# Kernel optimization log

Measured on AMD Instinct MI355X. Metric: run time of the kernel, lower is better.

Reference implementation:

```python
import jax, jax.numpy as jnp
import numpy as np

N_NODES = 50000
D = 128
N_EDGES = 600000


def setup_inputs() -> dict:
    key = jax.random.key(0)
    k_h, k_u, k_v, k_s, k_d = jax.random.split(key, 5)
    H = jax.random.normal(k_h, (N_NODES, D), dtype=jnp.float32)
    U = jax.random.normal(k_u, (D, D), dtype=jnp.float32)
    V = jax.random.normal(k_v, (D, D), dtype=jnp.float32)
    edge_src = jax.random.randint(k_s, (N_EDGES,), 0, N_NODES, dtype=jnp.int32)
    edge_dst = jax.random.randint(k_d, (N_EDGES,), 0, N_NODES, dtype=jnp.int32)
    return {"H": H, "U": U, "V": V, "edge_src": edge_src, "edge_dst": edge_dst}


def reference(H, U, V, edge_src, edge_dst):
    # Synchronous form of: new_rep[n] = relu(rep[n] @ U + sum_{m in N(n)} rep[m] @ V)
    # Compute H @ V once (one dense GEMM), then irregular gather by edge_src
    # and segment-sum scatter into destination nodes.
    hv = H @ V                                    # [N, D]
    msgs = jnp.take(hv, edge_src, axis=0)         # [E, D] irregular gather
    agg = jax.ops.segment_sum(msgs, edge_dst, num_segments=H.shape[0])  # [N, D]
    return jax.nn.relu(H @ U + agg)               # [N, D]
```

## Files before the change

### kernel.cpp

```cpp
#include <hip/hip_runtime.h>
#include <hip/hip_bf16.h>

constexpr int kNodes  = 50000;
constexpr int kEdges  = 600000;
constexpr int kD      = 128;
constexpr int kStrips = kNodes / 16;
constexpr int kStride = 64;

constexpr int kNB        = 400;
constexpr int kNPB       = 125;
constexpr int kEPB       = 4096;
constexpr int kBktBlocks = (kEdges + kEPB - 1) / kEPB;
constexpr int kCellCap   = 32;
constexpr int kCellStr   = 148;
constexpr int kPackBlocks  = 128;
constexpr int kPrepBlocks  = kBktBlocks + kPackBlocks;
constexpr int kGemmBlocks  = 768;
constexpr int kK2Blocks    = kNB + kGemmBlocks;

typedef __attribute__((ext_vector_type(8))) short  short8;
typedef __attribute__((ext_vector_type(4))) float  f32x4;

__device__ __forceinline__ unsigned short f2bfu(float x) {
    __hip_bfloat16 h = __float2bfloat16(x);
    return (unsigned short)__builtin_bit_cast(short, h);
}
__device__ __forceinline__ short f2bf(float x) {
    return __builtin_bit_cast(short, __float2bfloat16(x));
}

__global__ __launch_bounds__(256) void prep(const float* __restrict__ U,
                                            const float* __restrict__ V,
                                            const int* __restrict__ esrc,
                                            const int* __restrict__ edst,
                                            short* __restrict__ BTf,
                                            unsigned short* __restrict__ cnt_arr,
                                            unsigned int* __restrict__ barr) {
    const int bid = blockIdx.x;

    if (bid < kBktBlocks) {
        __shared__ int cur[kNB];
        for (int i = threadIdx.x; i < kNB; i += 256) cur[i] = 0;
        __syncthreads();

        const int e0 = bid * kEPB;
        int myd[16], mys[16];
#pragma unroll
        for (int i = 0; i < 16; ++i) {
            const int e = e0 + i * 256 + (int)threadIdx.x;
            myd[i] = (e < kEdges) ? edst[e] : -1;
            mys[i] = (e < kEdges) ? esrc[e] : 0;
        }
#pragma unroll
        for (int i = 0; i < 16; ++i) {
            if (myd[i] >= 0) {
                const int b = myd[i] / kNPB;
                const int slot = atomicAdd(&cur[b], 1);
                if (slot < kCellCap)
                    barr[((size_t)bid * kNB + b) * kCellCap + slot] =
                        ((unsigned)(myd[i] - b * kNPB) << 16) | (unsigned)mys[i];
            }
        }
        __syncthreads();
        for (int i = threadIdx.x; i < kNB; i += 256)
            cnt_arr[(size_t)i * kCellStr + bid] =
                (unsigned short)min(cur[i], kCellCap);
        return;
    }

    const int g = (bid - kBktBlocks) * 256 + (int)threadIdx.x;
    const int c = g >> 7;
    const int k = g & 127;
    const float x = (c < kD) ? U[k * kD + c] : V[k * kD + (c - kD)];
    const int q  = c >> 6;
    const int n  = (c >> 4) & 3;
    const int m  = c & 15;
    const int t  = k >> 5;
    const int kg = (k >> 3) & 3;
    const int ko = k & 7;
    const int lane = kg * 16 + m;
    BTf[((((q * 4 + n) * 4 + t) * 64 + lane) << 3) + ko] = f2bf(x);
}

__global__ __launch_bounds__(256) void gemm_sort(const float* __restrict__ H,
                                                 const short* __restrict__ BTf,
                                                 const unsigned short* __restrict__ cnt_arr,
                                                 const unsigned int* __restrict__ barr,
                                                 unsigned short* __restrict__ outb,
                                                 unsigned short* __restrict__ hvb,
                                                 int* __restrict__ cursor,
                                                 unsigned short* __restrict__ csr16) {
    const int bid = blockIdx.x;

    if (bid < kNB) {
        __shared__ int cnt[kNPB];
        for (int i = threadIdx.x; i < kNPB; i += 256) cnt[i] = 0;
        __syncthreads();

        const int b = bid;
        const int t = (int)threadIdx.x;
        if (t < kBktBlocks) {
            const int c = cnt_arr[(size_t)b * kCellStr + t];
            const unsigned int* cell = barr + ((size_t)t * kNB + b) * kCellCap;
            for (int j = 0; j < c; ++j) {
                const unsigned int p = cell[j];
                const int dl  = (int)(p >> 16);
                const int src = (int)(p & 0xffffu);
                const int slot = atomicAdd(&cnt[dl], 1);
                if (slot < kStride)
                    csr16[((size_t)b * kNPB + dl) * kStride + slot] = (unsigned short)src;
            }
        }
        __syncthreads();
        for (int i = threadIdx.x; i < kNPB; i += 256)
            cursor[b * kNPB + i] = cnt[i];
        return;
    }

    const int g  = bid - kNB;
    const int s0 = (int)((long)g       * kStrips / kGemmBlocks);
    const int s1 = (int)((long)(g + 1) * kStrips / kGemmBlocks);
    const int quad = threadIdx.x >> 6;
    const int lane = threadIdx.x & 63;
    const int m  = lane & 15;
    const int kg = lane >> 4;

    const short8* bq = reinterpret_cast<const short8*>(BTf)
                     + ((size_t)quad * 16) * 64 + lane;
    short8 bf[4][4];
#pragma unroll
    for (int n = 0; n < 4; ++n)
#pragma unroll
        for (int t = 0; t < 4; ++t)
            bf[n][t] = bq[(n * 4 + t) * 64];

    auto load_ha = [&](int s, float4 (&ha)[4][2]) {
        const float* hbase = H + ((long)s * 16 + m) * kD + kg * 8;
#pragma unroll
        for (int t = 0; t < 4; ++t) {
            ha[t][0] = *reinterpret_cast<const float4*>(hbase + t * 32);
            ha[t][1] = *reinterpret_cast<const float4*>(hbase + t * 32 + 4);
        }
    };

    auto compute_store = [&](int s, float4 (&ha)[4][2]) {
        short8 a[4];
#pragma unroll
        for (int t = 0; t < 4; ++t) {
            a[t][0] = f2bf(ha[t][0].x); a[t][1] = f2bf(ha[t][0].y);
            a[t][2] = f2bf(ha[t][0].z); a[t][3] = f2bf(ha[t][0].w);
            a[t][4] = f2bf(ha[t][1].x); a[t][5] = f2bf(ha[t][1].y);
            a[t][6] = f2bf(ha[t][1].z); a[t][7] = f2bf(ha[t][1].w);
        }

        f32x4 acc[4];
#pragma unroll
        for (int i = 0; i < 4; ++i) acc[i] = (f32x4){0.f, 0.f, 0.f, 0.f};
#pragma unroll
        for (int t = 0; t < 4; ++t)
#pragma unroll
            for (int n = 0; n < 4; ++n)
                acc[n] = __builtin_amdgcn_mfma_f32_16x16x32_bf16(bf[n][t], a[t], acc[n], 0, 0, 0);

        const long row0 = (long)s * 16;
        if (quad < 2) {
            unsigned short* rowp = outb + (size_t)(row0 + m) * 256 + quad * 64 + kg * 4;
#pragma unroll
            for (int n = 0; n < 4; ++n) {
                uint2 pk;
                pk.x = ((unsigned)f2bfu(acc[n][1]) << 16) | f2bfu(acc[n][0]);
                pk.y = ((unsigned)f2bfu(acc[n][3]) << 16) | f2bfu(acc[n][2]);
                *reinterpret_cast<uint2*>(rowp + n * 16) = pk;
            }
        } else {
            unsigned short* rowp = hvb + (size_t)(row0 + m) * kD + (quad - 2) * 64 + kg * 4;
#pragma unroll
            for (int n = 0; n < 4; ++n) {
                uint2 pk;
                pk.x = ((unsigned)f2bfu(acc[n][1]) << 16) | f2bfu(acc[n][0]);
                pk.y = ((unsigned)f2bfu(acc[n][3]) << 16) | f2bfu(acc[n][2]);
                *reinterpret_cast<uint2*>(rowp + n * 16) = pk;
            }
        }
    };

    float4 haA[4][2], haB[4][2];
    int s = s0;
    if (s >= s1) return;
    load_ha(s, haA);
    for (; s + 1 < s1; s += 2) {
        load_ha(s + 1, haB);
        compute_store(s, haA);
        if (s + 2 < s1) load_ha(s + 2, haA);
        compute_store(s + 1, haB);
    }
    if (s < s1) compute_store(s, haA);
}

__global__ __launch_bounds__(256) void aggregate_relu(const unsigned int* __restrict__ hvb,
                                                      const int* __restrict__ cursor,
                                                      const unsigned short* __restrict__ csr16,
                                                      float* __restrict__ out) {
    const int wid  = (int)((blockIdx.x * (long)blockDim.x + threadIdx.x) >> 6);
    const int lane = threadIdx.x & 63;
    if (wid >= kNodes) return;

    const unsigned int hw = reinterpret_cast<const unsigned int*>(out)[(size_t)wid * 128 + lane];
    const int deg = min(cursor[wid], kStride);
    const unsigned int w =
        reinterpret_cast<const unsigned int*>(csr16 + (size_t)wid * kStride)[lane & 31];

    float a0 = 0.f, a1 = 0.f;
    int e = 0;
    for (; e + 8 <= deg; e += 8) {
        const int p0 = __builtin_amdgcn_readlane(w, (e >> 1));
        const int p1 = __builtin_amdgcn_readlane(w, (e >> 1) + 1);
        const int p2 = __builtin_amdgcn_readlane(w, (e >> 1) + 2);
        const int p3 = __builtin_amdgcn_readlane(w, (e >> 1) + 3);
        const unsigned int w0 = hvb[(size_t)(p0 & 0xffff) * 64 + lane];
        const unsigned int w1 = hvb[(size_t)((p0 >> 16) & 0xffff) * 64 + lane];
        const unsigned int w2 = hvb[(size_t)(p1 & 0xffff) * 64 + lane];
        const unsigned int w3 = hvb[(size_t)((p1 >> 16) & 0xffff) * 64 + lane];
        const unsigned int w4 = hvb[(size_t)(p2 & 0xffff) * 64 + lane];
        const unsigned int w5 = hvb[(size_t)((p2 >> 16) & 0xffff) * 64 + lane];
        const unsigned int w6 = hvb[(size_t)(p3 & 0xffff) * 64 + lane];
        const unsigned int w7 = hvb[(size_t)((p3 >> 16) & 0xffff) * 64 + lane];
        a0 += __uint_as_float(w0 << 16) + __uint_as_float(w1 << 16)
            + __uint_as_float(w2 << 16) + __uint_as_float(w3 << 16)
            + __uint_as_float(w4 << 16) + __uint_as_float(w5 << 16)
            + __uint_as_float(w6 << 16) + __uint_as_float(w7 << 16);
        a1 += __uint_as_float(w0 & 0xffff0000u) + __uint_as_float(w1 & 0xffff0000u)
            + __uint_as_float(w2 & 0xffff0000u) + __uint_as_float(w3 & 0xffff0000u)
            + __uint_as_float(w4 & 0xffff0000u) + __uint_as_float(w5 & 0xffff0000u)
            + __uint_as_float(w6 & 0xffff0000u) + __uint_as_float(w7 & 0xffff0000u);
    }
    for (; e + 4 <= deg; e += 4) {
        const int p0 = __builtin_amdgcn_readlane(w, e >> 1);
        const int p1 = __builtin_amdgcn_readlane(w, (e >> 1) + 1);
        const unsigned int w0 = hvb[(size_t)(p0 & 0xffff) * 64 + lane];
        const unsigned int w1 = hvb[(size_t)((p0 >> 16) & 0xffff) * 64 + lane];
        const unsigned int w2 = hvb[(size_t)(p1 & 0xffff) * 64 + lane];
        const unsigned int w3 = hvb[(size_t)((p1 >> 16) & 0xffff) * 64 + lane];
        a0 += __uint_as_float(w0 << 16) + __uint_as_float(w1 << 16)
            + __uint_as_float(w2 << 16) + __uint_as_float(w3 << 16);
        a1 += __uint_as_float(w0 & 0xffff0000u) + __uint_as_float(w1 & 0xffff0000u)
            + __uint_as_float(w2 & 0xffff0000u) + __uint_as_float(w3 & 0xffff0000u);
    }
    for (; e < deg; ++e) {
        const int p = __builtin_amdgcn_readlane(w, e >> 1);
        const int s = (e & 1) ? ((p >> 16) & 0xffff) : (p & 0xffff);
        const unsigned int wv = hvb[(size_t)s * 64 + lane];
        a0 += __uint_as_float(wv << 16);
        a1 += __uint_as_float(wv & 0xffff0000u);
    }

    const float b0 = __uint_as_float(hw << 16);
    const float b1 = __uint_as_float(hw & 0xffff0000u);

    float2* out2 = reinterpret_cast<float2*>(out);
    float2 o;
    o.x = fmaxf(b0 + a0, 0.f);
    o.y = fmaxf(b1 + a1, 0.f);
    out2[(size_t)wid * 64 + lane] = o;
}

extern "C" void kernel_launch(void* const* d_in, const int* in_sizes, int n_in,
                              void* d_out, int out_size, void* d_ws, size_t ws_size,
                              hipStream_t stream) {
    const float* H    = (const float*)d_in[0];
    const float* U    = (const float*)d_in[1];
    const float* V    = (const float*)d_in[2];
    const int*   esrc = (const int*)d_in[3];
    const int*   edst = (const int*)d_in[4];

    float* out = (float*)d_out;

    char* p = (char*)d_ws;
    unsigned short* hvb     = (unsigned short*)p;  p += (size_t)kNodes * kD * 2;
    short*          BTf     = (short*)p;           p += (size_t)256 * kD * 2;
    unsigned short* cnt_arr = (unsigned short*)p;  p += (size_t)kNB * kCellStr * 2;
    unsigned int*   barr    = (unsigned int*)p;    p += (size_t)kBktBlocks * kNB * kCellCap * 4;
    int*            cursor  = (int*)p;             p += (size_t)kNodes * 4;
    unsigned short* csr16   = (unsigned short*)p;  p += (size_t)kNodes * kStride * 2;

    prep<<<kPrepBlocks, 256, 0, stream>>>(U, V, esrc, edst, BTf, cnt_arr, barr);

    gemm_sort<<<kK2Blocks, 256, 0, stream>>>(H, BTf, cnt_arr, barr,
                                             (unsigned short*)d_out, hvb, cursor, csr16);

    aggregate_relu<<<(kNodes * 64 + 255) / 256, 256, 0, stream>>>(
        (const unsigned int*)hvb, cursor, csr16, out);
}
```

Baseline: 63.42 us.

## Fuse pipeline into two kernels: GEMM+bucketing, then in-LDS sort+aggregate

Cuts the pipeline from three launches to two. The GEMM blocks now convert U/V to bf16 fragments directly from fp32 global memory instead of using a separate prepacked weight buffer, and they share a launch with the edge-bucketing blocks. The per-bucket sort now builds each destination's neighbor list in shared memory inside a 1024-thread aggregation block, removing the global CSR and cursor round-trip. In exchange, every GEMM block re-reads and re-converts the weights with strided loads, and aggregation runs only 400 large blocks, which may lower occupancy and load balance.

```diff
diff --git a/kernel.cpp b/kernel.cpp
--- a/kernel.cpp
+++ b/kernel.cpp
@@ -5,7 +5,6 @@
 constexpr int kEdges  = 600000;
 constexpr int kD      = 128;
 constexpr int kStrips = kNodes / 16;
-constexpr int kStride = 64;
 
 constexpr int kNB        = 400;
 constexpr int kNPB       = 125;
@@ -13,10 +12,9 @@
 constexpr int kBktBlocks = (kEdges + kEPB - 1) / kEPB;
 constexpr int kCellCap   = 32;
 constexpr int kCellStr   = 148;
-constexpr int kPackBlocks  = 128;
-constexpr int kPrepBlocks  = kBktBlocks + kPackBlocks;
+constexpr int kListCap   = 64;
 constexpr int kGemmBlocks  = 768;
-constexpr int kK2Blocks    = kNB + kGemmBlocks;
+constexpr int kK1Blocks    = kBktBlocks + kGemmBlocks;
 
 typedef __attribute__((ext_vector_type(8))) short  short8;
 typedef __attribute__((ext_vector_type(4))) float  f32x4;
@@ -29,13 +27,15 @@
     return __builtin_bit_cast(short, __float2bfloat16(x));
 }
 
-__global__ __launch_bounds__(256) void prep(const float* __restrict__ U,
-                                            const float* __restrict__ V,
-                                            const int* __restrict__ esrc,
-                                            const int* __restrict__ edst,
-                                            short* __restrict__ BTf,
-                                            unsigned short* __restrict__ cnt_arr,
-                                            unsigned int* __restrict__ barr) {
+__global__ __launch_bounds__(256) void gemm_bucket(const float* __restrict__ H,
+                                                   const float* __restrict__ U,
+                                                   const float* __restrict__ V,
+                                                   const int* __restrict__ esrc,
+                                                   const int* __restrict__ edst,
+                                                   unsigned short* __restrict__ outb,
+                                                   unsigned short* __restrict__ hvb,
+                                                   unsigned short* __restrict__ cnt_arr,
+                                                   unsigned int* __restrict__ barr) {
     const int bid = blockIdx.x;
 
     if (bid < kBktBlocks) {
@@ -68,56 +68,7 @@
         return;
     }
 
-    const int g = (bid - kBktBlocks) * 256 + (int)threadIdx.x;
-    const int c = g >> 7;
-    const int k = g & 127;
-    const float x = (c < kD) ? U[k * kD + c] : V[k * kD + (c - kD)];
-    const int q  = c >> 6;
-    const int n  = (c >> 4) & 3;
-    const int m  = c & 15;
-    const int t  = k >> 5;
-    const int kg = (k >> 3) & 3;
-    const int ko = k & 7;
-    const int lane = kg * 16 + m;
-    BTf[((((q * 4 + n) * 4 + t) * 64 + lane) << 3) + ko] = f2bf(x);
-}
-
-__global__ __launch_bounds__(256) void gemm_sort(const float* __restrict__ H,
-                                                 const short* __restrict__ BTf,
-                                                 const unsigned short* __restrict__ cnt_arr,
-                                                 const unsigned int* __restrict__ barr,
-                                                 unsigned short* __restrict__ outb,
-                                                 unsigned short* __restrict__ hvb,
-                                                 int* __restrict__ cursor,
-                                                 unsigned short* __restrict__ csr16) {
-    const int bid = blockIdx.x;
-
-    if (bid < kNB) {
-        __shared__ int cnt[kNPB];
-        for (int i = threadIdx.x; i < kNPB; i += 256) cnt[i] = 0;
-        __syncthreads();
-
-        const int b = bid;
-        const int t = (int)threadIdx.x;
-        if (t < kBktBlocks) {
-            const int c = cnt_arr[(size_t)b * kCellStr + t];
-            const unsigned int* cell = barr + ((size_t)t * kNB + b) * kCellCap;
-            for (int j = 0; j < c; ++j) {
-                const unsigned int p = cell[j];
-                const int dl  = (int)(p >> 16);
-                const int src = (int)(p & 0xffffu);
-                const int slot = atomicAdd(&cnt[dl], 1);
-                if (slot < kStride)
-                    csr16[((size_t)b * kNPB + dl) * kStride + slot] = (unsigned short)src;
-            }
-        }
-        __syncthreads();
-        for (int i = threadIdx.x; i < kNPB; i += 256)
-            cursor[b * kNPB + i] = cnt[i];
-        return;
-    }
-
-    const int g  = bid - kNB;
+    const int g  = bid - kBktBlocks;
     const int s0 = (int)((long)g       * kStrips / kGemmBlocks);
     const int s1 = (int)((long)(g + 1) * kStrips / kGemmBlocks);
     const int quad = threadIdx.x >> 6;
@@ -125,14 +76,17 @@
     const int m  = lane & 15;
     const int kg = lane >> 4;
 
-    const short8* bq = reinterpret_cast<const short8*>(BTf)
-                     + ((size_t)quad * 16) * 64 + lane;
+    const float* W = (quad < 2) ? U : V;
+    const int cb = (quad & 1) * 64 + m;
     short8 bf[4][4];
 #pragma unroll
     for (int n = 0; n < 4; ++n)
 #pragma unroll
-        for (int t = 0; t < 4; ++t)
-            bf[n][t] = bq[(n * 4 + t) * 64];
+        for (int t = 0; t < 4; ++t) {
+#pragma unroll
+            for (int j = 0; j < 8; ++j)
+                bf[n][t][j] = f2bf(W[(size_t)(t * 32 + kg * 8 + j) * kD + cb + n * 16]);
+        }
 
     auto load_ha = [&](int s, float4 (&ha)[4][2]) {
         const float* hbase = H + ((long)s * 16 + m) * kD + kg * 8;
@@ -197,71 +151,96 @@
     if (s < s1) compute_store(s, haA);
 }
 
-__global__ __launch_bounds__(256) void aggregate_relu(const unsigned int* __restrict__ hvb,
-                                                      const int* __restrict__ cursor,
-                                                      const unsigned short* __restrict__ csr16,
-                                                      float* __restrict__ out) {
-    const int wid  = (int)((blockIdx.x * (long)blockDim.x + threadIdx.x) >> 6);
-    const int lane = threadIdx.x & 63;
-    if (wid >= kNodes) return;
-
-    const unsigned int hw = reinterpret_cast<const unsigned int*>(out)[(size_t)wid * 128 + lane];
-    const int deg = min(cursor[wid], kStride);
-    const unsigned int w =
-        reinterpret_cast<const unsigned int*>(csr16 + (size_t)wid * kStride)[lane & 31];
-
-    float a0 = 0.f, a1 = 0.f;
-    int e = 0;
-    for (; e + 8 <= deg; e += 8) {
-        const int p0 = __builtin_amdgcn_readlane(w, (e >> 1));
-        const int p1 = __builtin_amdgcn_readlane(w, (e >> 1) + 1);
-        const int p2 = __builtin_amdgcn_readlane(w, (e >> 1) + 2);
-        const int p3 = __builtin_amdgcn_readlane(w, (e >> 1) + 3);
-        const unsigned int w0 = hvb[(size_t)(p0 & 0xffff) * 64 + lane];
-        const unsigned int w1 = hvb[(size_t)((p0 >> 16) & 0xffff) * 64 + lane];
-        const unsigned int w2 = hvb[(size_t)(p1 & 0xffff) * 64 + lane];
-        const unsigned int w3 = hvb[(size_t)((p1 >> 16) & 0xffff) * 64 + lane];
-        const unsigned int w4 = hvb[(size_t)(p2 & 0xffff) * 64 + lane];
-        const unsigned int w5 = hvb[(size_t)((p2 >> 16) & 0xffff) * 64 + lane];
-        const unsigned int w6 = hvb[(size_t)(p3 & 0xffff) * 64 + lane];
-        const unsigned int w7 = hvb[(size_t)((p3 >> 16) & 0xffff) * 64 + lane];
-        a0 += __uint_as_float(w0 << 16) + __uint_as_float(w1 << 16)
-            + __uint_as_float(w2 << 16) + __uint_as_float(w3 << 16)
-            + __uint_as_float(w4 << 16) + __uint_as_float(w5 << 16)
-            + __uint_as_float(w6 << 16) + __uint_as_float(w7 << 16);
-        a1 += __uint_as_float(w0 & 0xffff0000u) + __uint_as_float(w1 & 0xffff0000u)
-            + __uint_as_float(w2 & 0xffff0000u) + __uint_as_float(w3 & 0xffff0000u)
-            + __uint_as_float(w4 & 0xffff0000u) + __uint_as_float(w5 & 0xffff0000u)
-            + __uint_as_float(w6 & 0xffff0000u) + __uint_as_float(w7 & 0xffff0000u);
-    }
-    for (; e + 4 <= deg; e += 4) {
-        const int p0 = __builtin_amdgcn_readlane(w, e >> 1);
-        const int p1 = __builtin_amdgcn_readlane(w, (e >> 1) + 1);
-        const unsigned int w0 = hvb[(size_t)(p0 & 0xffff) * 64 + lane];
-        const unsigned int w1 = hvb[(size_t)((p0 >> 16) & 0xffff) * 64 + lane];
-        const unsigned int w2 = hvb[(size_t)(p1 & 0xffff) * 64 + lane];
-        const unsigned int w3 = hvb[(size_t)((p1 >> 16) & 0xffff) * 64 + lane];
-        a0 += __uint_as_float(w0 << 16) + __uint_as_float(w1 << 16)
-            + __uint_as_float(w2 << 16) + __uint_as_float(w3 << 16);
-        a1 += __uint_as_float(w0 & 0xffff0000u) + __uint_as_float(w1 & 0xffff0000u)
-            + __uint_as_float(w2 & 0xffff0000u) + __uint_as_float(w3 & 0xffff0000u);
-    }
-    for (; e < deg; ++e) {
-        const int p = __builtin_amdgcn_readlane(w, e >> 1);
-        const int s = (e & 1) ? ((p >> 16) & 0xffff) : (p & 0xffff);
-        const unsigned int wv = hvb[(size_t)s * 64 + lane];
-        a0 += __uint_as_float(wv << 16);
-        a1 += __uint_as_float(wv & 0xffff0000u);
-    }
-
-    const float b0 = __uint_as_float(hw << 16);
-    const float b1 = __uint_as_float(hw & 0xffff0000u);
-
-    float2* out2 = reinterpret_cast<float2*>(out);
-    float2 o;
-    o.x = fmaxf(b0 + a0, 0.f);
-    o.y = fmaxf(b1 + a1, 0.f);
-    out2[(size_t)wid * 64 + lane] = o;
+__global__ __launch_bounds__(1024) void sort_aggregate(const unsigned int* __restrict__ hvb,
+                                                       const unsigned short* __restrict__ cnt_arr,
+                                                       const unsigned int* __restrict__ barr,
+                                                       float* __restrict__ out) {
+    __shared__ unsigned short list16[kNPB * kListCap];
+    __shared__ int cnt[kNPB];
+    const int b = blockIdx.x;
+
+    for (int i = threadIdx.x; i < kNPB; i += 1024) cnt[i] = 0;
+    __syncthreads();
+
+    const int t = (int)threadIdx.x;
+    if (t < kBktBlocks) {
+        const int c = cnt_arr[(size_t)b * kCellStr + t];
+        const unsigned int* cell = barr + ((size_t)t * kNB + b) * kCellCap;
+        for (int j = 0; j < c; ++j) {
+            const unsigned int p = cell[j];
+            const int dl  = (int)(p >> 16);
+            const int src = (int)(p & 0xffffu);
+            const int slot = atomicAdd(&cnt[dl], 1);
+            if (slot < kListCap)
+                list16[dl * kListCap + slot] = (unsigned short)src;
+        }
+    }
+    __syncthreads();
+
+    const unsigned int* list32 = reinterpret_cast<const unsigned int*>(list16);
+    const int wave = (int)threadIdx.x >> 6;
+    const int lane = (int)threadIdx.x & 63;
+    const int n0 = b * kNPB;
+
+    for (int dl = wave; dl < kNPB; dl += 16) {
+        const int deg = min(cnt[dl], kListCap);
+        const unsigned int w = list32[dl * 32 + (lane & 31)];
+
+        const unsigned int hw =
+            reinterpret_cast<const unsigned int*>(out)[(size_t)(n0 + dl) * 128 + lane];
+
+        float a0 = 0.f, a1 = 0.f;
+        int e = 0;
+        for (; e + 8 <= deg; e += 8) {
+            const int p0 = __builtin_amdgcn_readlane(w, (e >> 1));
+            const int p1 = __builtin_amdgcn_readlane(w, (e >> 1) + 1);
+            const int p2 = __builtin_amdgcn_readlane(w, (e >> 1) + 2);
+            const int p3 = __builtin_amdgcn_readlane(w, (e >> 1) + 3);
+            const unsigned int w0 = hvb[(size_t)(p0 & 0xffff) * 64 + lane];
+            const unsigned int w1 = hvb[(size_t)((p0 >> 16) & 0xffff) * 64 + lane];
+            const unsigned int w2 = hvb[(size_t)(p1 & 0xffff) * 64 + lane];
+            const unsigned int w3 = hvb[(size_t)((p1 >> 16) & 0xffff) * 64 + lane];
+            const unsigned int w4 = hvb[(size_t)(p2 & 0xffff) * 64 + lane];
+            const unsigned int w5 = hvb[(size_t)((p2 >> 16) & 0xffff) * 64 + lane];
+            const unsigned int w6 = hvb[(size_t)(p3 & 0xffff) * 64 + lane];
+            const unsigned int w7 = hvb[(size_t)((p3 >> 16) & 0xffff) * 64 + lane];
+            a0 += __uint_as_float(w0 << 16) + __uint_as_float(w1 << 16)
+                + __uint_as_float(w2 << 16) + __uint_as_float(w3 << 16)
+                + __uint_as_float(w4 << 16) + __uint_as_float(w5 << 16)
+                + __uint_as_float(w6 << 16) + __uint_as_float(w7 << 16);
+            a1 += __uint_as_float(w0 & 0xffff0000u) + __uint_as_float(w1 & 0xffff0000u)
+                + __uint_as_float(w2 & 0xffff0000u) + __uint_as_float(w3 & 0xffff0000u)
+                + __uint_as_float(w4 & 0xffff0000u) + __uint_as_float(w5 & 0xffff0000u)
+                + __uint_as_float(w6 & 0xffff0000u) + __uint_as_float(w7 & 0xffff0000u);
+        }
+        for (; e + 4 <= deg; e += 4) {
+            const int p0 = __builtin_amdgcn_readlane(w, e >> 1);
+            const int p1 = __builtin_amdgcn_readlane(w, (e >> 1) + 1);
+            const unsigned int w0 = hvb[(size_t)(p0 & 0xffff) * 64 + lane];
+            const unsigned int w1 = hvb[(size_t)((p0 >> 16) & 0xffff) * 64 + lane];
+            const unsigned int w2 = hvb[(size_t)(p1 & 0xffff) * 64 + lane];
+            const unsigned int w3 = hvb[(size_t)((p1 >> 16) & 0xffff) * 64 + lane];
+            a0 += __uint_as_float(w0 << 16) + __uint_as_float(w1 << 16)
+                + __uint_as_float(w2 << 16) + __uint_as_float(w3 << 16);
+            a1 += __uint_as_float(w0 & 0xffff0000u) + __uint_as_float(w1 & 0xffff0000u)
+                + __uint_as_float(w2 & 0xffff0000u) + __uint_as_float(w3 & 0xffff0000u);
+        }
+        for (; e < deg; ++e) {
+            const int p = __builtin_amdgcn_readlane(w, e >> 1);
+            const int s = (e & 1) ? ((p >> 16) & 0xffff) : (p & 0xffff);
+            const unsigned int wv = hvb[(size_t)s * 64 + lane];
+            a0 += __uint_as_float(wv << 16);
+            a1 += __uint_as_float(wv & 0xffff0000u);
+        }
+
+        const float b0 = __uint_as_float(hw << 16);
+        const float b1 = __uint_as_float(hw & 0xffff0000u);
+
+        float2 o;
+        o.x = fmaxf(b0 + a0, 0.f);
+        o.y = fmaxf(b1 + a1, 0.f);
+        reinterpret_cast<float2*>(out)[(size_t)(n0 + dl) * 64 + lane] = o;
+    }
 }
 
 extern "C" void kernel_launch(void* const* d_in, const int* in_sizes, int n_in,
@@ -277,17 +256,11 @@
 
     char* p = (char*)d_ws;
     unsigned short* hvb     = (unsigned short*)p;  p += (size_t)kNodes * kD * 2;
-    short*          BTf     = (short*)p;           p += (size_t)256 * kD * 2;
     unsigned short* cnt_arr = (unsigned short*)p;  p += (size_t)kNB * kCellStr * 2;
     unsigned int*   barr    = (unsigned int*)p;    p += (size_t)kBktBlocks * kNB * kCellCap * 4;
-    int*            cursor  = (int*)p;             p += (size_t)kNodes * 4;
-    unsigned short* csr16   = (unsigned short*)p;  p += (size_t)kNodes * kStride * 2;
-
-    prep<<<kPrepBlocks, 256, 0, stream>>>(U, V, esrc, edst, BTf, cnt_arr, barr);
-
-    gemm_sort<<<kK2Blocks, 256, 0, stream>>>(H, BTf, cnt_arr, barr,
-                                             (unsigned short*)d_out, hvb, cursor, csr16);
-
-    aggregate_relu<<<(kNodes * 64 + 255) / 256, 256, 0, stream>>>(
-        (const unsigned int*)hvb, cursor, csr16, out);
-}
+
+    gemm_bucket<<<kK1Blocks, 256, 0, stream>>>(H, U, V, esrc, edst,
+                                               (unsigned short*)d_out, hvb, cnt_arr, barr);
+
+    sort_aggregate<<<kNB, 1024, 0, stream>>>((const unsigned int*)hvb, cnt_arr, barr, out);
+}
```

Result: faster. 61.40 us (-3.2%).
